# Optimization experiments

Measured on AMD Instinct MI355X. Metric: run time of the kernel, lower is better.

## Reference

```python
import jax, jax.numpy as jnp
import numpy as np

K = 1024
DIM = 64
DECAY = 0.99
EPS = 1e-05
CC = 0.25


def setup_inputs() -> dict:
    key = jax.random.key(0)
    k1, k2 = jax.random.split(key)
    inputs = jax.random.normal(k1, (32, DIM, 64, 64), dtype=jnp.float32)
    # embedding initialized uniform(-1/K, 1/K); ema_w starts as a copy
    emb_w = jax.random.uniform(k2, (K, DIM), dtype=jnp.float32, minval=-1.0 / K, maxval=1.0 / K)
    ema_w = emb_w
    ema_cluster_size = jnp.zeros((K,), dtype=jnp.float32)
    return {"inputs": inputs, "emb_w": emb_w, "ema_cluster_size": ema_cluster_size, "ema_w": ema_w}


def reference(inputs, emb_w, ema_cluster_size, ema_w):
    # NCHW -> NHWC
    x = jnp.transpose(inputs, (0, 2, 3, 1))  # [B,H,W,D]
    B, H, W, D = x.shape
    flat = x.reshape(-1, D)  # [N,D]
    # squared L2 distances: |f|^2 - 2 f.W^T + |w|^2
    d = (jnp.sum(flat * flat, axis=1, keepdims=True)
         - 2.0 * flat @ emb_w.T
         + jnp.sum(emb_w * emb_w, axis=1)[None, :])  # [N,K]
    idx = jnp.argmin(d, axis=1)  # [N]
    encodings = idx.reshape(B, H, W)
    quantized = emb_w[idx].reshape(B, H, W, D)

    # training-mode EMA update (matches one_hot.sum(0) and one_hot.T @ flatten)
    counts = jax.ops.segment_sum(jnp.ones_like(idx, dtype=jnp.float32), idx, num_segments=K)
    new_cs = ema_cluster_size * DECAY + (1.0 - DECAY) * counts
    n = jnp.sum(new_cs)
    new_cs = (new_cs + EPS) / (n + K * EPS) * n
    dw = jax.ops.segment_sum(flat, idx, num_segments=K)  # [K,D]
    new_ema_w = ema_w * DECAY + (1.0 - DECAY) * dw
    new_emb_w = new_ema_w / new_cs[:, None]

    e_latent_loss = jnp.mean((quantized - x) ** 2)  # both terms equal in value
    loss = e_latent_loss + CC * e_latent_loss
    # straight-through (value-equal in fwd)
    q_out = jnp.transpose(quantized, (0, 3, 1, 2))  # NHWC -> NCHW
    nll = jnp.ones((1,), dtype=jnp.float32)
    return q_out, encodings, loss, nll, new_cs, new_ema_w, new_emb_w
```

## Files before the change

kernel.cpp:

```cpp
#include <hip/hip_runtime.h>
#include <math.h>

#define KCODES 1024
#define DIMV   64
#define NROWS  131072
#define HWSZ   4096
#define NELEM  8388608
#define CAP    224
#define CANDCAP 1024


typedef __attribute__((ext_vector_type(8))) short bf16x8;
typedef __attribute__((ext_vector_type(4))) float f32x4;

static __device__ __forceinline__ unsigned short f2bf(float x) {
    unsigned int u = __float_as_uint(x);
    unsigned int r = (u + 0x7FFFu + ((u >> 16) & 1u)) >> 16;
    return (unsigned short)r;
}

__global__ __launch_bounds__(64) void vq_prep3_kernel(
    const float* __restrict__ emb, float* __restrict__ s_w,
    unsigned short* __restrict__ WB, unsigned int* __restrict__ wmax_bits)
{
    int k = blockIdx.x, t = threadIdx.x;
    float v = emb[k * DIMV + t];

    {
        int cg = k >> 4, n = k & 15;
        int kh = t >> 5, q = (t & 31) >> 3, j = t & 7;
        WB[((cg * 2 + kh) * 4 + q) * 128 + n * 8 + j] = f2bf(v);
    }

    float av = fabsf(v);
    #pragma unroll
    for (int off = 32; off > 0; off >>= 1)
        av = fmaxf(av, __shfl_down(av, off, 64));
    if (t == 0) atomicMax(wmax_bits, __float_as_uint(av));

    __shared__ float sv[64];
    __shared__ float sr[8];
    sv[t] = v;
    __syncthreads();
    if (t < 8) {
        float x = sv[t];
        float sq = x * x;
        asm("" : "+v"(sq));
        float r = sq;
        #pragma unroll
        for (int m = 1; m < 8; ++m) {
            float y = sv[8 * m + t];
            float s2 = y * y;
            asm("" : "+v"(s2));
            r += s2;
        }
        sr[t] = r;
    }
    __syncthreads();
    if (t == 0)
        s_w[k] = ((sr[0] + sr[1]) + (sr[2] + sr[3])) + ((sr[4] + sr[5]) + (sr[6] + sr[7]));
}

__global__ __launch_bounds__(256, 4) void vq_assign_kernel(
    const float* __restrict__ inp, const float* __restrict__ emb,
    const unsigned short* __restrict__ WB, const float* __restrict__ s_w,
    const unsigned int* __restrict__ wmax_bits,
    float* __restrict__ tmp_flat, float* __restrict__ enc_out,
    double* __restrict__ loss_sum, int* __restrict__ counts,
    int* __restrict__ rowlist)
{
    __shared__ float At[128 * 65];
    __shared__ float sfL[128];
    __shared__ float errL[128];
    __shared__ unsigned long long rowBest[128];
    __shared__ int bkL[128];
    __shared__ int candL[CANDCAP];
    __shared__ int candCnt;

    const int t = threadIdx.x;
    const int n0 = blockIdx.x * 128;
    const int bq  = n0 >> 12;
    const int hw0 = n0 & 4095;
    const float* fin = inp + (size_t)bq * (DIMV * HWSZ) + hw0;

    if (t < 128) rowBest[t] = ~0ULL;
    if (t == 0) candCnt = 0;

    #pragma unroll
    for (int j = 0; j < 8; ++j) {
        int id = j * 256 + t;
        int i = id >> 5;
        int c4 = id & 31;
        float4 v = *(const float4*)(fin + (size_t)i * HWSZ + 4 * c4);
        int r = 4 * c4;
        At[(r + 0) * 65 + i] = v.x + v.x;  At[(r + 1) * 65 + i] = v.y + v.y;
        At[(r + 2) * 65 + i] = v.z + v.z;  At[(r + 3) * 65 + i] = v.w + v.w;
    }
    __syncthreads();

    if (t < 128) {
        const float* gr = &At[t * 65];
        float r8[8];
        #pragma unroll
        for (int j = 0; j < 8; ++j) {
            float h = 0.5f * gr[j];
            float sq = h * h;
            asm("" : "+v"(sq));
            r8[j] = sq;
        }
        #pragma unroll
        for (int m = 1; m < 8; ++m) {
            #pragma unroll
            for (int j = 0; j < 8; ++j) {
                float h = 0.5f * gr[8 * m + j];
                float sq = h * h;
                asm("" : "+v"(sq));
                r8[j] += sq;
            }
        }
        sfL[t] = ((r8[0] + r8[1]) + (r8[2] + r8[3])) + ((r8[4] + r8[5]) + (r8[6] + r8[7]));
        float S = 0.0f;
        #pragma unroll
        for (int i = 0; i < 64; ++i) S += fabsf(gr[i]);
        float wmax = __uint_as_float(*wmax_bits);
        errL[t] = fmaf(S * wmax, 0.015625f, 2e-5f);
    }
    __syncthreads();

    const int wv = t >> 6, l = t & 63;
    const int m = l & 15, q = l >> 4;
    bf16x8 afr[2][2];
    float sfr[2][4];
    float erf[2][4];
    #pragma unroll
    for (int rg2 = 0; rg2 < 2; ++rg2) {
        int row = (2 * wv + rg2) * 16 + m;
        const float* gr = &At[row * 65];
        #pragma unroll
        for (int kh = 0; kh < 2; ++kh) {
            bf16x8 a;
            #pragma unroll
            for (int j = 0; j < 8; ++j)
                a[j] = (short)f2bf(gr[kh * 32 + q * 8 + j]);
            afr[rg2][kh] = a;
        }
        #pragma unroll
        for (int reg = 0; reg < 4; ++reg) {
            sfr[rg2][reg] = sfL[(2 * wv + rg2) * 16 + q * 4 + reg];
            erf[rg2][reg] = errL[(2 * wv + rg2) * 16 + q * 4 + reg];
        }
    }

    const unsigned short* wbq = WB + q * 128 + m * 8;
    const float* swm = s_w + m;

    float mn[2][4];
    #pragma unroll
    for (int rg2 = 0; rg2 < 2; ++rg2)
        #pragma unroll
        for (int reg = 0; reg < 4; ++reg) mn[rg2][reg] = 3.0e38f;

    {
        bf16x8 pa0 = *(const bf16x8*)(wbq);
        bf16x8 pa1 = *(const bf16x8*)(wbq + 512);
        float   swa = swm[0];
        bf16x8 pb0 = *(const bf16x8*)(wbq + 1024);
        bf16x8 pb1 = *(const bf16x8*)(wbq + 1024 + 512);
        float   swb = swm[16];
        for (int cg = 0; cg < 64; cg += 2) {
            #pragma unroll
            for (int rg2 = 0; rg2 < 2; ++rg2) {
                f32x4 acc = {0.f, 0.f, 0.f, 0.f};
                acc = __builtin_amdgcn_mfma_f32_16x16x32_bf16(afr[rg2][0], pa0, acc, 0, 0, 0);
                acc = __builtin_amdgcn_mfma_f32_16x16x32_bf16(afr[rg2][1], pa1, acc, 0, 0, 0);
                #pragma unroll
                for (int reg = 0; reg < 4; ++reg) {
                    float dt = (sfr[rg2][reg] - acc[reg]) + swa;
                    mn[rg2][reg] = fminf(mn[rg2][reg], dt);
                }
            }
            int cna = cg + 2 <= 62 ? cg + 2 : 62;
            pa0 = *(const bf16x8*)(wbq + cna * 1024);
            pa1 = *(const bf16x8*)(wbq + cna * 1024 + 512);
            swa = swm[cna * 16];
            #pragma unroll
            for (int rg2 = 0; rg2 < 2; ++rg2) {
                f32x4 acc = {0.f, 0.f, 0.f, 0.f};
                acc = __builtin_amdgcn_mfma_f32_16x16x32_bf16(afr[rg2][0], pb0, acc, 0, 0, 0);
                acc = __builtin_amdgcn_mfma_f32_16x16x32_bf16(afr[rg2][1], pb1, acc, 0, 0, 0);
                #pragma unroll
                for (int reg = 0; reg < 4; ++reg) {
                    float dt = (sfr[rg2][reg] - acc[reg]) + swb;
                    mn[rg2][reg] = fminf(mn[rg2][reg], dt);
                }
            }
            int cnb = cg + 3 <= 63 ? cg + 3 : 63;
            pb0 = *(const bf16x8*)(wbq + cnb * 1024);
            pb1 = *(const bf16x8*)(wbq + cnb * 1024 + 512);
            swb = swm[cnb * 16];
        }
    }

    float th[2][4];
    #pragma unroll
    for (int rg2 = 0; rg2 < 2; ++rg2)
        #pragma unroll
        for (int reg = 0; reg < 4; ++reg) {
            float v = mn[rg2][reg];
            v = fminf(v, __shfl_xor(v, 1, 64));
            v = fminf(v, __shfl_xor(v, 2, 64));
            v = fminf(v, __shfl_xor(v, 4, 64));
            v = fminf(v, __shfl_xor(v, 8, 64));
            th[rg2][reg] = v + erf[rg2][reg];
        }

    {
        bf16x8 pa0 = *(const bf16x8*)(wbq);
        bf16x8 pa1 = *(const bf16x8*)(wbq + 512);
        float   swa = swm[0];
        bf16x8 pb0 = *(const bf16x8*)(wbq + 1024);
        bf16x8 pb1 = *(const bf16x8*)(wbq + 1024 + 512);
        float   swb = swm[16];
        for (int cg = 0; cg < 64; cg += 2) {
            #pragma unroll
            for (int rg2 = 0; rg2 < 2; ++rg2) {
                f32x4 acc = {0.f, 0.f, 0.f, 0.f};
                acc = __builtin_amdgcn_mfma_f32_16x16x32_bf16(afr[rg2][0], pa0, acc, 0, 0, 0);
                acc = __builtin_amdgcn_mfma_f32_16x16x32_bf16(afr[rg2][1], pa1, acc, 0, 0, 0);
                #pragma unroll
                for (int reg = 0; reg < 4; ++reg) {
                    float dt = (sfr[rg2][reg] - acc[reg]) + swa;
                    if (dt <= th[rg2][reg]) {
                        int row = (2 * wv + rg2) * 16 + q * 4 + reg;
                        int p = atomicAdd(&candCnt, 1);
                        if (p < CANDCAP) candL[p] = (row << 10) | (cg * 16 + m);
                    }
                }
            }
            int cna = cg + 2 <= 62 ? cg + 2 : 62;
            pa0 = *(const bf16x8*)(wbq + cna * 1024);
            pa1 = *(const bf16x8*)(wbq + cna * 1024 + 512);
            swa = swm[cna * 16];
            #pragma unroll
            for (int rg2 = 0; rg2 < 2; ++rg2) {
                f32x4 acc = {0.f, 0.f, 0.f, 0.f};
                acc = __builtin_amdgcn_mfma_f32_16x16x32_bf16(afr[rg2][0], pb0, acc, 0, 0, 0);
                acc = __builtin_amdgcn_mfma_f32_16x16x32_bf16(afr[rg2][1], pb1, acc, 0, 0, 0);
                #pragma unroll
                for (int reg = 0; reg < 4; ++reg) {
                    float dt = (sfr[rg2][reg] - acc[reg]) + swb;
                    if (dt <= th[rg2][reg]) {
                        int row = (2 * wv + rg2) * 16 + q * 4 + reg;
                        int p = atomicAdd(&candCnt, 1);
                        if (p < CANDCAP) candL[p] = (row << 10) | ((cg + 1) * 16 + m);
                    }
                }
            }
            int cnb = cg + 3 <= 63 ? cg + 3 : 63;
            pb0 = *(const bf16x8*)(wbq + cnb * 1024);
            pb1 = *(const bf16x8*)(wbq + cnb * 1024 + 512);
            swb = swm[cnb * 16];
        }
    }
    __syncthreads();

    int nc = candCnt < CANDCAP ? candCnt : CANDCAP;
    for (int c = t; c < nc; c += 256) {
        int pk = candL[c];
        int r = pk >> 10, k = pk & 1023;
        const float* wk = emb + (size_t)k * DIMV;
        const float* gr = &At[r * 65];
        float acc = 0.0f;
        #pragma unroll
        for (int i = 0; i < DIMV; ++i)
            acc = __builtin_fmaf(gr[i], wk[i], acc);
        float d = (sfL[r] - acc) + s_w[k];
        unsigned int u = __float_as_uint(d);
        unsigned int s = (u & 0x80000000u) ? ~u : (u | 0x80000000u);
        unsigned long long key = ((unsigned long long)s << 32) | (unsigned int)k;
        atomicMin(&rowBest[r], key);
    }
    __syncthreads();

    if (t < 128 && (rowBest[t] == ~0ULL || candCnt > CANDCAP)) {
        int r = t;
        const float* gr = &At[r * 65];
        float bd = 3.0e38f; int bk = 0;
        for (int k = 0; k < KCODES; ++k) {
            const float* wk = emb + (size_t)k * DIMV;
            float acc = 0.0f;
            #pragma unroll
            for (int i = 0; i < DIMV; ++i)
                acc = __builtin_fmaf(gr[i], wk[i], acc);
            float d = (sfL[r] - acc) + s_w[k];
            if (d < bd) { bd = d; bk = k; }
        }
        unsigned int u = __float_as_uint(bd);
        unsigned int s = (u & 0x80000000u) ? ~u : (u | 0x80000000u);
        rowBest[r] = ((unsigned long long)s << 32) | (unsigned int)bk;
    }
    __syncthreads();

    if (t < 128) {
        int r = t;
        int bk = (int)(rowBest[r] & 1023ULL);
        enc_out[n0 + r] = (float)bk;
        bkL[r] = bk;
        int pos = atomicAdd(&counts[bk], 1);
        if (pos < CAP) rowlist[bk * CAP + pos] = n0 + r;
    }
    __syncthreads();

    float* tq = tmp_flat + (size_t)n0 * DIMV;
    double lsum = 0.0;
    #pragma unroll
    for (int j = 0; j < 32; ++j) {
        int idx = j * 256 + t;
        int r = idx >> 6;
        int i = idx & 63;
        int bk = bkL[r];
        float fi = 0.5f * At[r * 65 + i];
        tq[r * DIMV + i] = fi;
        float qv = emb[bk * DIMV + i];
        double dq = (double)qv - (double)fi;
        lsum = fma(dq, dq, lsum);
    }
    #pragma unroll
    for (int off = 32; off > 0; off >>= 1)
        lsum += __shfl_down(lsum, off, 64);
    if ((t & 63) == 0) atomicAdd(loss_sum, lsum);
}

__global__ __launch_bounds__(256) void vq_dw_all_kernel(
    const float* __restrict__ tmp_flat, const int* __restrict__ rowlist,
    const int* __restrict__ counts, const float* __restrict__ ema_cs,
    const float* __restrict__ ema_w, const double* __restrict__ loss_sum,
    float* __restrict__ out_loss, float* __restrict__ out_nll,
    float* __restrict__ out_ncs, float* __restrict__ out_nema,
    float* __restrict__ out_nemb)
{
    const int k = blockIdx.x;
    const int t = threadIdx.x;
    const double DECAY = 0.99;
    const double OMD   = 1.0 - 0.99;
    const double EPSV  = 1e-5;

    __shared__ double sm[256];
    double part = 0.0;
    #pragma unroll
    for (int j0 = 0; j0 < 4; ++j0) {
        int j = j0 * 256 + t;
        part += (double)ema_cs[j] * DECAY + OMD * (double)counts[j];
    }
    sm[t] = part;
    __syncthreads();
    #pragma unroll
    for (int off = 128; off > 0; off >>= 1) {
        if (t < off) sm[t] += sm[t + off];
        __syncthreads();
    }
    double nsum = sm[0];

    int cnt = counts[k];
    double ncs = (double)ema_cs[k] * DECAY + OMD * (double)cnt;
    double adj = (ncs + EPSV) / (nsum + (double)KCODES * EPSV) * nsum;
    if (t == 0) out_ncs[k] = (float)adj;
    if (k == 0 && t == 0) {
        double e = loss_sum[0] / (double)NELEM;
        out_loss[0] = (float)(e + 0.25 * e);
        out_nll[0]  = 1.0f;
    }

    int i = t & 63;
    int sub = t >> 6;
    int cap = cnt < CAP ? cnt : CAP;

    float acc = 0.0f;
    for (int r = sub; r < cap; r += 4) {
        int n = rowlist[k * CAP + r];
        acc += tmp_flat[(size_t)n * DIMV + i];
    }

    __shared__ float red[256];
    red[t] = acc;
    __syncthreads();
    if (t < 128) red[t] += red[t + 128];
    __syncthreads();
    if (t < 64) {
        float dwv = red[t] + red[t + 64];
        int idx = k * DIMV + i;
        double ne = (double)ema_w[idx] * DECAY + OMD * (double)dwv;
        out_nema[idx] = (float)ne;
        out_nemb[idx] = (float)(ne / adj);
    }
}

__global__ __launch_bounds__(256) void vq_qout_kernel(
    const float* __restrict__ enc, const float* __restrict__ emb,
    float* __restrict__ q_out)
{
    __shared__ int bkL[128];
    const int t = threadIdx.x;
    const int n0 = blockIdx.x * 128;
    const int bq  = n0 >> 12;
    const int hw0 = n0 & 4095;
    if (t < 128) bkL[t] = (int)enc[n0 + t];
    __syncthreads();
    float* qo = q_out + (size_t)bq * (DIMV * HWSZ) + hw0;
    #pragma unroll
    for (int j = 0; j < 32; ++j) {
        int idx = j * 256 + t;
        int r = idx & 127;
        int i = idx >> 7;
        qo[(size_t)i * HWSZ + r] = emb[bkL[r] * DIMV + i];
    }
}

extern "C" void kernel_launch(void* const* d_in, const int* in_sizes, int n_in,
                              void* d_out, int out_size, void* d_ws, size_t ws_size,
                              hipStream_t stream) {
    const float* inp    = (const float*)d_in[0];
    const float* emb    = (const float*)d_in[1];
    const float* ema_cs = (const float*)d_in[2];
    const float* ema_w  = (const float*)d_in[3];

    char* ws = (char*)d_ws;
    double*         loss_sum  = (double*)(ws + 0);
    unsigned int*   wmax_bits = (unsigned int*)(ws + 16);
    int*            counts    = (int*)(ws + 32);
    float*          s_w       = (float*)(ws + 4128);
    unsigned short* WB        = (unsigned short*)(ws + 8224);
    int*            rowlist   = (int*)(ws + 139296);

    float* out       = (float*)d_out;
    float* q_out     = out;
    float* enc_out   = out + 8388608;
    float* out_loss  = out + 8519680;
    float* out_nll   = out + 8519681;
    float* out_ncs   = out + 8519682;
    float* out_nema  = out + 8520706;
    float* out_nemb  = out + 8586242;

    hipMemsetAsync(ws, 0, 4128, stream);
    hipLaunchKernelGGL(vq_prep3_kernel, dim3(KCODES), dim3(64), 0, stream,
                       emb, s_w, WB, wmax_bits);
    hipLaunchKernelGGL(vq_assign_kernel, dim3(NROWS / 128), dim3(256), 0, stream,
                       inp, emb, WB, s_w, wmax_bits,
                       q_out , enc_out, loss_sum, counts, rowlist);
    hipLaunchKernelGGL(vq_dw_all_kernel, dim3(KCODES), dim3(256), 0, stream,
                       q_out , rowlist, counts, ema_cs, ema_w, loss_sum,
                       out_loss, out_nll, out_ncs, out_nema, out_nemb);
    hipLaunchKernelGGL(vq_qout_kernel, dim3(NROWS / 128), dim3(256), 0, stream,
                       enc_out, emb, q_out);
}
```

Baseline: 278.8 us.

## Halve rows per block in VQ assign kernel and drop per-row norm from distance

The assign kernel now handles 64 rows per block instead of 128, with each wave owning a single 16-row MFMA tile. This halves the A-fragment and min registers and lets the launch bound ask for 8 blocks per CU. The row norm |f|^2 is removed from the per-code distance compare, since it is constant per row and does not change the argmin or the threshold test. The candidate buffer shrinks, and the dw gather loop gets an unroll hint. The trade-off is that every block now reloads the full codebook for half as many rows, doubling codebook traffic through L2.

```diff
diff --git a/kernel.cpp b/kernel.cpp
--- a/kernel.cpp
+++ b/kernel.cpp
@@ -7,7 +7,8 @@
 #define HWSZ   4096
 #define NELEM  8388608
 #define CAP    224
-#define CANDCAP 1024
+#define CANDCAP 384
+#define RPB    64
 
 
 typedef __attribute__((ext_vector_type(8))) short bf16x8;
@@ -61,7 +62,7 @@
         s_w[k] = ((sr[0] + sr[1]) + (sr[2] + sr[3])) + ((sr[4] + sr[5]) + (sr[6] + sr[7]));
 }
 
-__global__ __launch_bounds__(256, 4) void vq_assign_kernel(
+__global__ __launch_bounds__(256, 8) void vq_assign_kernel(
     const float* __restrict__ inp, const float* __restrict__ emb,
     const unsigned short* __restrict__ WB, const float* __restrict__ s_w,
     const unsigned int* __restrict__ wmax_bits,
@@ -69,28 +70,28 @@
     double* __restrict__ loss_sum, int* __restrict__ counts,
     int* __restrict__ rowlist)
 {
-    __shared__ float At[128 * 65];
-    __shared__ float sfL[128];
-    __shared__ float errL[128];
-    __shared__ unsigned long long rowBest[128];
-    __shared__ int bkL[128];
+    __shared__ float At[RPB * 65];
+    __shared__ float sfL[RPB];
+    __shared__ float errL[RPB];
+    __shared__ unsigned long long rowBest[RPB];
+    __shared__ int bkL[RPB];
     __shared__ int candL[CANDCAP];
     __shared__ int candCnt;
 
     const int t = threadIdx.x;
-    const int n0 = blockIdx.x * 128;
+    const int n0 = blockIdx.x * RPB;
     const int bq  = n0 >> 12;
     const int hw0 = n0 & 4095;
     const float* fin = inp + (size_t)bq * (DIMV * HWSZ) + hw0;
 
-    if (t < 128) rowBest[t] = ~0ULL;
+    if (t < RPB) rowBest[t] = ~0ULL;
     if (t == 0) candCnt = 0;
 
     #pragma unroll
-    for (int j = 0; j < 8; ++j) {
+    for (int j = 0; j < 4; ++j) {
         int id = j * 256 + t;
-        int i = id >> 5;
-        int c4 = id & 31;
+        int i = id >> 4;
+        int c4 = id & 15;
         float4 v = *(const float4*)(fin + (size_t)i * HWSZ + 4 * c4);
         int r = 4 * c4;
         At[(r + 0) * 65 + i] = v.x + v.x;  At[(r + 1) * 65 + i] = v.y + v.y;
@@ -98,7 +99,7 @@
     }
     __syncthreads();
 
-    if (t < 128) {
+    if (t < RPB) {
         const float* gr = &At[t * 65];
         float r8[8];
         #pragma unroll
@@ -129,36 +130,22 @@
 
     const int wv = t >> 6, l = t & 63;
     const int m = l & 15, q = l >> 4;
-    bf16x8 afr[2][2];
-    float sfr[2][4];
-    float erf[2][4];
-    #pragma unroll
-    for (int rg2 = 0; rg2 < 2; ++rg2) {
-        int row = (2 * wv + rg2) * 16 + m;
+    bf16x8 a0, a1;
+    {
+        int row = wv * 16 + m;
         const float* gr = &At[row * 65];
         #pragma unroll
-        for (int kh = 0; kh < 2; ++kh) {
-            bf16x8 a;
-            #pragma unroll
-            for (int j = 0; j < 8; ++j)
-                a[j] = (short)f2bf(gr[kh * 32 + q * 8 + j]);
-            afr[rg2][kh] = a;
-        }
-        #pragma unroll
-        for (int reg = 0; reg < 4; ++reg) {
-            sfr[rg2][reg] = sfL[(2 * wv + rg2) * 16 + q * 4 + reg];
-            erf[rg2][reg] = errL[(2 * wv + rg2) * 16 + q * 4 + reg];
-        }
+        for (int j = 0; j < 8; ++j) a0[j] = (short)f2bf(gr[q * 8 + j]);
+        #pragma unroll
+        for (int j = 0; j < 8; ++j) a1[j] = (short)f2bf(gr[32 + q * 8 + j]);
     }
 
     const unsigned short* wbq = WB + q * 128 + m * 8;
     const float* swm = s_w + m;
 
-    float mn[2][4];
-    #pragma unroll
-    for (int rg2 = 0; rg2 < 2; ++rg2)
-        #pragma unroll
-        for (int reg = 0; reg < 4; ++reg) mn[rg2][reg] = 3.0e38f;
+    float mn[4];
+    #pragma unroll
+    for (int reg = 0; reg < 4; ++reg) mn[reg] = 3.0e38f;
 
     {
         bf16x8 pa0 = *(const bf16x8*)(wbq);
@@ -168,51 +155,43 @@
         bf16x8 pb1 = *(const bf16x8*)(wbq + 1024 + 512);
         float   swb = swm[16];
         for (int cg = 0; cg < 64; cg += 2) {
-            #pragma unroll
-            for (int rg2 = 0; rg2 < 2; ++rg2) {
+            {
                 f32x4 acc = {0.f, 0.f, 0.f, 0.f};
-                acc = __builtin_amdgcn_mfma_f32_16x16x32_bf16(afr[rg2][0], pa0, acc, 0, 0, 0);
-                acc = __builtin_amdgcn_mfma_f32_16x16x32_bf16(afr[rg2][1], pa1, acc, 0, 0, 0);
+                acc = __builtin_amdgcn_mfma_f32_16x16x32_bf16(a0, pa0, acc, 0, 0, 0);
+                acc = __builtin_amdgcn_mfma_f32_16x16x32_bf16(a1, pa1, acc, 0, 0, 0);
                 #pragma unroll
-                for (int reg = 0; reg < 4; ++reg) {
-                    float dt = (sfr[rg2][reg] - acc[reg]) + swa;
-                    mn[rg2][reg] = fminf(mn[rg2][reg], dt);
-                }
+                for (int reg = 0; reg < 4; ++reg)
+                    mn[reg] = fminf(mn[reg], swa - acc[reg]);
             }
-            int cna = cg + 2 <= 62 ? cg + 2 : 62;
+            int cna = (cg + 2) & 63;
             pa0 = *(const bf16x8*)(wbq + cna * 1024);
             pa1 = *(const bf16x8*)(wbq + cna * 1024 + 512);
             swa = swm[cna * 16];
-            #pragma unroll
-            for (int rg2 = 0; rg2 < 2; ++rg2) {
+            {
                 f32x4 acc = {0.f, 0.f, 0.f, 0.f};
-                acc = __builtin_amdgcn_mfma_f32_16x16x32_bf16(afr[rg2][0], pb0, acc, 0, 0, 0);
-                acc = __builtin_amdgcn_mfma_f32_16x16x32_bf16(afr[rg2][1], pb1, acc, 0, 0, 0);
+                acc = __builtin_amdgcn_mfma_f32_16x16x32_bf16(a0, pb0, acc, 0, 0, 0);
+                acc = __builtin_amdgcn_mfma_f32_16x16x32_bf16(a1, pb1, acc, 0, 0, 0);
                 #pragma unroll
-                for (int reg = 0; reg < 4; ++reg) {
-                    float dt = (sfr[rg2][reg] - acc[reg]) + swb;
-                    mn[rg2][reg] = fminf(mn[rg2][reg], dt);
-                }
+                for (int reg = 0; reg < 4; ++reg)
+                    mn[reg] = fminf(mn[reg], swb - acc[reg]);
             }
-            int cnb = cg + 3 <= 63 ? cg + 3 : 63;
+            int cnb = (cg + 3) & 63;
             pb0 = *(const bf16x8*)(wbq + cnb * 1024);
             pb1 = *(const bf16x8*)(wbq + cnb * 1024 + 512);
             swb = swm[cnb * 16];
         }
     }
 
-    float th[2][4];
-    #pragma unroll
-    for (int rg2 = 0; rg2 < 2; ++rg2)
-        #pragma unroll
-        for (int reg = 0; reg < 4; ++reg) {
-            float v = mn[rg2][reg];
-            v = fminf(v, __shfl_xor(v, 1, 64));
-            v = fminf(v, __shfl_xor(v, 2, 64));
-            v = fminf(v, __shfl_xor(v, 4, 64));
-            v = fminf(v, __shfl_xor(v, 8, 64));
-            th[rg2][reg] = v + erf[rg2][reg];
-        }
+    float th[4];
+    #pragma unroll
+    for (int reg = 0; reg < 4; ++reg) {
+        float v = mn[reg];
+        v = fminf(v, __shfl_xor(v, 1, 64));
+        v = fminf(v, __shfl_xor(v, 2, 64));
+        v = fminf(v, __shfl_xor(v, 4, 64));
+        v = fminf(v, __shfl_xor(v, 8, 64));
+        th[reg] = v + errL[wv * 16 + q * 4 + reg];
+    }
 
     {
         bf16x8 pa0 = *(const bf16x8*)(wbq);
@@ -222,41 +201,37 @@
         bf16x8 pb1 = *(const bf16x8*)(wbq + 1024 + 512);
         float   swb = swm[16];
         for (int cg = 0; cg < 64; cg += 2) {
-            #pragma unroll
-            for (int rg2 = 0; rg2 < 2; ++rg2) {
+            {
                 f32x4 acc = {0.f, 0.f, 0.f, 0.f};
-                acc = __builtin_amdgcn_mfma_f32_16x16x32_bf16(afr[rg2][0], pa0, acc, 0, 0, 0);
-                acc = __builtin_amdgcn_mfma_f32_16x16x32_bf16(afr[rg2][1], pa1, acc, 0, 0, 0);
+                acc = __builtin_amdgcn_mfma_f32_16x16x32_bf16(a0, pa0, acc, 0, 0, 0);
+                acc = __builtin_amdgcn_mfma_f32_16x16x32_bf16(a1, pa1, acc, 0, 0, 0);
                 #pragma unroll
                 for (int reg = 0; reg < 4; ++reg) {
-                    float dt = (sfr[rg2][reg] - acc[reg]) + swa;
-                    if (dt <= th[rg2][reg]) {
-                        int row = (2 * wv + rg2) * 16 + q * 4 + reg;
+                    if (swa - acc[reg] <= th[reg]) {
+                        int row = wv * 16 + q * 4 + reg;
                         int p = atomicAdd(&candCnt, 1);
                         if (p < CANDCAP) candL[p] = (row << 10) | (cg * 16 + m);
                     }
                 }
             }
-            int cna = cg + 2 <= 62 ? cg + 2 : 62;
+            int cna = (cg + 2) & 63;
             pa0 = *(const bf16x8*)(wbq + cna * 1024);
             pa1 = *(const bf16x8*)(wbq + cna * 1024 + 512);
             swa = swm[cna * 16];
-            #pragma unroll
-            for (int rg2 = 0; rg2 < 2; ++rg2) {
+            {
                 f32x4 acc = {0.f, 0.f, 0.f, 0.f};
-                acc = __builtin_amdgcn_mfma_f32_16x16x32_bf16(afr[rg2][0], pb0, acc, 0, 0, 0);
-                acc = __builtin_amdgcn_mfma_f32_16x16x32_bf16(afr[rg2][1], pb1, acc, 0, 0, 0);
+                acc = __builtin_amdgcn_mfma_f32_16x16x32_bf16(a0, pb0, acc, 0, 0, 0);
+                acc = __builtin_amdgcn_mfma_f32_16x16x32_bf16(a1, pb1, acc, 0, 0, 0);
                 #pragma unroll
                 for (int reg = 0; reg < 4; ++reg) {
-                    float dt = (sfr[rg2][reg] - acc[reg]) + swb;
-                    if (dt <= th[rg2][reg]) {
-                        int row = (2 * wv + rg2) * 16 + q * 4 + reg;
+                    if (swb - acc[reg] <= th[reg]) {
+                        int row = wv * 16 + q * 4 + reg;
                         int p = atomicAdd(&candCnt, 1);
                         if (p < CANDCAP) candL[p] = (row << 10) | ((cg + 1) * 16 + m);
                     }
                 }
             }
-            int cnb = cg + 3 <= 63 ? cg + 3 : 63;
+            int cnb = (cg + 3) & 63;
             pb0 = *(const bf16x8*)(wbq + cnb * 1024);
             pb1 = *(const bf16x8*)(wbq + cnb * 1024 + 512);
             swb = swm[cnb * 16];
@@ -282,7 +257,7 @@
     }
     __syncthreads();
 
-    if (t < 128 && (rowBest[t] == ~0ULL || candCnt > CANDCAP)) {
+    if (t < RPB && (rowBest[t] == ~0ULL || candCnt > CANDCAP)) {
         int r = t;
         const float* gr = &At[r * 65];
         float bd = 3.0e38f; int bk = 0;
@@ -301,7 +276,7 @@
     }
     __syncthreads();
 
-    if (t < 128) {
+    if (t < RPB) {
         int r = t;
         int bk = (int)(rowBest[r] & 1023ULL);
         enc_out[n0 + r] = (float)bk;
@@ -314,7 +289,7 @@
     float* tq = tmp_flat + (size_t)n0 * DIMV;
     double lsum = 0.0;
     #pragma unroll
-    for (int j = 0; j < 32; ++j) {
+    for (int j = 0; j < 16; ++j) {
         int idx = j * 256 + t;
         int r = idx >> 6;
         int i = idx & 63;
@@ -376,6 +351,7 @@
     int cap = cnt < CAP ? cnt : CAP;
 
     float acc = 0.0f;
+    #pragma unroll 4
     for (int r = sub; r < cap; r += 4) {
         int n = rowlist[k * CAP + r];
         acc += tmp_flat[(size_t)n * DIMV + i];
@@ -444,7 +420,7 @@
     hipMemsetAsync(ws, 0, 4128, stream);
     hipLaunchKernelGGL(vq_prep3_kernel, dim3(KCODES), dim3(64), 0, stream,
                        emb, s_w, WB, wmax_bits);
-    hipLaunchKernelGGL(vq_assign_kernel, dim3(NROWS / 128), dim3(256), 0, stream,
+    hipLaunchKernelGGL(vq_assign_kernel, dim3(NROWS / RPB), dim3(256), 0, stream,
                        inp, emb, WB, s_w, wmax_bits,
                        q_out , enc_out, loss_sum, counts, rowlist);
     hipLaunchKernelGGL(vq_dw_all_kernel, dim3(KCODES), dim3(256), 0, stream,
```

Measured after the change: 334.9 us. 20.1% more time.

## Stage codebook tiles through double-buffered LDS in VQ assign kernel

Applied to the files above, without the earlier changes.

Replaces per-lane global loads of the bf16 codebook with cooperative block-wide staging into a double-buffered LDS tile, prefetching the next tile into registers during MFMA work. Also caches the code-norm vector in LDS and drops the per-row |f|^2 term from the min-search, since it is constant per row and does not change the argmin. The extra LDS lowers the occupancy hint from 4 to 3 blocks per CU and adds two barriers per tile pair. The dw kernel also gets an unroll pragma.

```diff
diff --git a/kernel.cpp b/kernel.cpp
--- a/kernel.cpp
+++ b/kernel.cpp
@@ -8,6 +8,7 @@
 #define NELEM  8388608
 #define CAP    224
 #define CANDCAP 1024
+#define RPB    128
 
 
 typedef __attribute__((ext_vector_type(8))) short bf16x8;
@@ -61,7 +62,7 @@
         s_w[k] = ((sr[0] + sr[1]) + (sr[2] + sr[3])) + ((sr[4] + sr[5]) + (sr[6] + sr[7]));
 }
 
-__global__ __launch_bounds__(256, 4) void vq_assign_kernel(
+__global__ __launch_bounds__(256, 3) void vq_assign_kernel(
     const float* __restrict__ inp, const float* __restrict__ emb,
     const unsigned short* __restrict__ WB, const float* __restrict__ s_w,
     const unsigned int* __restrict__ wmax_bits,
@@ -69,22 +70,27 @@
     double* __restrict__ loss_sum, int* __restrict__ counts,
     int* __restrict__ rowlist)
 {
-    __shared__ float At[128 * 65];
-    __shared__ float sfL[128];
-    __shared__ float errL[128];
-    __shared__ unsigned long long rowBest[128];
-    __shared__ int bkL[128];
+    __shared__ float At[RPB * 65];
+    __shared__ float sWL[KCODES];
+    __shared__ __align__(16) unsigned short Bst[2][2048];
+    __shared__ float sfL[RPB];
+    __shared__ float errL[RPB];
+    __shared__ unsigned long long rowBest[RPB];
+    __shared__ int bkL[RPB];
     __shared__ int candL[CANDCAP];
     __shared__ int candCnt;
 
     const int t = threadIdx.x;
-    const int n0 = blockIdx.x * 128;
+    const int n0 = blockIdx.x * RPB;
     const int bq  = n0 >> 12;
     const int hw0 = n0 & 4095;
     const float* fin = inp + (size_t)bq * (DIMV * HWSZ) + hw0;
 
-    if (t < 128) rowBest[t] = ~0ULL;
+    if (t < RPB) rowBest[t] = ~0ULL;
     if (t == 0) candCnt = 0;
+
+    #pragma unroll
+    for (int j = 0; j < 4; ++j) sWL[j * 256 + t] = s_w[j * 256 + t];
 
     #pragma unroll
     for (int j = 0; j < 8; ++j) {
@@ -96,9 +102,17 @@
         At[(r + 0) * 65 + i] = v.x + v.x;  At[(r + 1) * 65 + i] = v.y + v.y;
         At[(r + 2) * 65 + i] = v.z + v.z;  At[(r + 3) * 65 + i] = v.w + v.w;
     }
-    __syncthreads();
-
-    if (t < 128) {
+
+    const uint4* wbsrc = (const uint4*)WB;
+    uint4 nx0, nx1;
+    {
+        uint4 st0 = wbsrc[t];
+        *(uint4*)&Bst[0][t * 8] = st0;
+        nx0 = wbsrc[256 + t];
+    }
+    __syncthreads();
+
+    if (t < RPB) {
         const float* gr = &At[t * 65];
         float r8[8];
         #pragma unroll
@@ -129,8 +143,8 @@
 
     const int wv = t >> 6, l = t & 63;
     const int m = l & 15, q = l >> 4;
+    const int lq = q * 128 + m * 8;
     bf16x8 afr[2][2];
-    float sfr[2][4];
     float erf[2][4];
     #pragma unroll
     for (int rg2 = 0; rg2 < 2; ++rg2) {
@@ -145,14 +159,9 @@
             afr[rg2][kh] = a;
         }
         #pragma unroll
-        for (int reg = 0; reg < 4; ++reg) {
-            sfr[rg2][reg] = sfL[(2 * wv + rg2) * 16 + q * 4 + reg];
+        for (int reg = 0; reg < 4; ++reg)
             erf[rg2][reg] = errL[(2 * wv + rg2) * 16 + q * 4 + reg];
-        }
-    }
-
-    const unsigned short* wbq = WB + q * 128 + m * 8;
-    const float* swm = s_w + m;
+    }
 
     float mn[2][4];
     #pragma unroll
@@ -160,45 +169,47 @@
         #pragma unroll
         for (int reg = 0; reg < 4; ++reg) mn[rg2][reg] = 3.0e38f;
 
-    {
-        bf16x8 pa0 = *(const bf16x8*)(wbq);
-        bf16x8 pa1 = *(const bf16x8*)(wbq + 512);
-        float   swa = swm[0];
-        bf16x8 pb0 = *(const bf16x8*)(wbq + 1024);
-        bf16x8 pb1 = *(const bf16x8*)(wbq + 1024 + 512);
-        float   swb = swm[16];
-        for (int cg = 0; cg < 64; cg += 2) {
+    #pragma unroll 1
+    for (int tp = 0; tp < 16; ++tp) {
+        int tt = 2 * tp;
+        nx1 = wbsrc[((tt + 2) & 31) * 256 + t];
+        #pragma unroll
+        for (int c = 0; c < 2; ++c) {
+            int cg = 2 * tt + c;
+            bf16x8 b0 = *(const bf16x8*)&Bst[0][c * 1024 + lq];
+            bf16x8 b1 = *(const bf16x8*)&Bst[0][c * 1024 + 512 + lq];
+            float sw = sWL[cg * 16 + m];
             #pragma unroll
             for (int rg2 = 0; rg2 < 2; ++rg2) {
                 f32x4 acc = {0.f, 0.f, 0.f, 0.f};
-                acc = __builtin_amdgcn_mfma_f32_16x16x32_bf16(afr[rg2][0], pa0, acc, 0, 0, 0);
-                acc = __builtin_amdgcn_mfma_f32_16x16x32_bf16(afr[rg2][1], pa1, acc, 0, 0, 0);
+                acc = __builtin_amdgcn_mfma_f32_16x16x32_bf16(afr[rg2][0], b0, acc, 0, 0, 0);
+                acc = __builtin_amdgcn_mfma_f32_16x16x32_bf16(afr[rg2][1], b1, acc, 0, 0, 0);
                 #pragma unroll
-                for (int reg = 0; reg < 4; ++reg) {
-                    float dt = (sfr[rg2][reg] - acc[reg]) + swa;
-                    mn[rg2][reg] = fminf(mn[rg2][reg], dt);
-                }
+                for (int reg = 0; reg < 4; ++reg)
+                    mn[rg2][reg] = fminf(mn[rg2][reg], sw - acc[reg]);
             }
-            int cna = cg + 2 <= 62 ? cg + 2 : 62;
-            pa0 = *(const bf16x8*)(wbq + cna * 1024);
-            pa1 = *(const bf16x8*)(wbq + cna * 1024 + 512);
-            swa = swm[cna * 16];
+        }
+        *(uint4*)&Bst[1][t * 8] = nx0;
+        __syncthreads();
+        nx0 = wbsrc[((tt + 3) & 31) * 256 + t];
+        #pragma unroll
+        for (int c = 0; c < 2; ++c) {
+            int cg = 2 * (tt + 1) + c;
+            bf16x8 b0 = *(const bf16x8*)&Bst[1][c * 1024 + lq];
+            bf16x8 b1 = *(const bf16x8*)&Bst[1][c * 1024 + 512 + lq];
+            float sw = sWL[cg * 16 + m];
             #pragma unroll
             for (int rg2 = 0; rg2 < 2; ++rg2) {
                 f32x4 acc = {0.f, 0.f, 0.f, 0.f};
-                acc = __builtin_amdgcn_mfma_f32_16x16x32_bf16(afr[rg2][0], pb0, acc, 0, 0, 0);
-                acc = __builtin_amdgcn_mfma_f32_16x16x32_bf16(afr[rg2][1], pb1, acc, 0, 0, 0);
+                acc = __builtin_amdgcn_mfma_f32_16x16x32_bf16(afr[rg2][0], b0, acc, 0, 0, 0);
+                acc = __builtin_amdgcn_mfma_f32_16x16x32_bf16(afr[rg2][1], b1, acc, 0, 0, 0);
                 #pragma unroll
-                for (int reg = 0; reg < 4; ++reg) {
-                    float dt = (sfr[rg2][reg] - acc[reg]) + swb;
-                    mn[rg2][reg] = fminf(mn[rg2][reg], dt);
-                }
+                for (int reg = 0; reg < 4; ++reg)
+                    mn[rg2][reg] = fminf(mn[rg2][reg], sw - acc[reg]);
             }
-            int cnb = cg + 3 <= 63 ? cg + 3 : 63;
-            pb0 = *(const bf16x8*)(wbq + cnb * 1024);
-            pb1 = *(const bf16x8*)(wbq + cnb * 1024 + 512);
-            swb = swm[cnb * 16];
-        }
+        }
+        *(uint4*)&Bst[0][t * 8] = nx1;
+        __syncthreads();
     }
 
     float th[2][4];
@@ -214,55 +225,58 @@
             th[rg2][reg] = v + erf[rg2][reg];
         }
 
-    {
-        bf16x8 pa0 = *(const bf16x8*)(wbq);
-        bf16x8 pa1 = *(const bf16x8*)(wbq + 512);
-        float   swa = swm[0];
-        bf16x8 pb0 = *(const bf16x8*)(wbq + 1024);
-        bf16x8 pb1 = *(const bf16x8*)(wbq + 1024 + 512);
-        float   swb = swm[16];
-        for (int cg = 0; cg < 64; cg += 2) {
+    #pragma unroll 1
+    for (int tp = 0; tp < 16; ++tp) {
+        int tt = 2 * tp;
+        nx1 = wbsrc[((tt + 2) & 31) * 256 + t];
+        #pragma unroll
+        for (int c = 0; c < 2; ++c) {
+            int cg = 2 * tt + c;
+            bf16x8 b0 = *(const bf16x8*)&Bst[0][c * 1024 + lq];
+            bf16x8 b1 = *(const bf16x8*)&Bst[0][c * 1024 + 512 + lq];
+            float sw = sWL[cg * 16 + m];
             #pragma unroll
             for (int rg2 = 0; rg2 < 2; ++rg2) {
                 f32x4 acc = {0.f, 0.f, 0.f, 0.f};
-                acc = __builtin_amdgcn_mfma_f32_16x16x32_bf16(afr[rg2][0], pa0, acc, 0, 0, 0);
-                acc = __builtin_amdgcn_mfma_f32_16x16x32_bf16(afr[rg2][1], pa1, acc, 0, 0, 0);
+                acc = __builtin_amdgcn_mfma_f32_16x16x32_bf16(afr[rg2][0], b0, acc, 0, 0, 0);
+                acc = __builtin_amdgcn_mfma_f32_16x16x32_bf16(afr[rg2][1], b1, acc, 0, 0, 0);
                 #pragma unroll
                 for (int reg = 0; reg < 4; ++reg) {
-                    float dt = (sfr[rg2][reg] - acc[reg]) + swa;
-                    if (dt <= th[rg2][reg]) {
+                    if (sw - acc[reg] <= th[rg2][reg]) {
                         int row = (2 * wv + rg2) * 16 + q * 4 + reg;
                         int p = atomicAdd(&candCnt, 1);
                         if (p < CANDCAP) candL[p] = (row << 10) | (cg * 16 + m);
                     }
                 }
             }
-            int cna = cg + 2 <= 62 ? cg + 2 : 62;
-            pa0 = *(const bf16x8*)(wbq + cna * 1024);
-            pa1 = *(const bf16x8*)(wbq + cna * 1024 + 512);
-            swa = swm[cna * 16];
+        }
+        *(uint4*)&Bst[1][t * 8] = nx0;
+        __syncthreads();
+        nx0 = wbsrc[((tt + 3) & 31) * 256 + t];
+        #pragma unroll
+        for (int c = 0; c < 2; ++c) {
+            int cg = 2 * (tt + 1) + c;
+            bf16x8 b0 = *(const bf16x8*)&Bst[1][c * 1024 + lq];
+            bf16x8 b1 = *(const bf16x8*)&Bst[1][c * 1024 + 512 + lq];
+            float sw = sWL[cg * 16 + m];
             #pragma unroll
             for (int rg2 = 0; rg2 < 2; ++rg2) {
                 f32x4 acc = {0.f, 0.f, 0.f, 0.f};
-                acc = __builtin_amdgcn_mfma_f32_16x16x32_bf16(afr[rg2][0], pb0, acc, 0, 0, 0);
-                acc = __builtin_amdgcn_mfma_f32_16x16x32_bf16(afr[rg2][1], pb1, acc, 0, 0, 0);
+                acc = __builtin_amdgcn_mfma_f32_16x16x32_bf16(afr[rg2][0], b0, acc, 0, 0, 0);
+                acc = __builtin_amdgcn_mfma_f32_16x16x32_bf16(afr[rg2][1], b1, acc, 0, 0, 0);
                 #pragma unroll
                 for (int reg = 0; reg < 4; ++reg) {
-                    float dt = (sfr[rg2][reg] - acc[reg]) + swb;
-                    if (dt <= th[rg2][reg]) {
+                    if (sw - acc[reg] <= th[rg2][reg]) {
                         int row = (2 * wv + rg2) * 16 + q * 4 + reg;
                         int p = atomicAdd(&candCnt, 1);
-                        if (p < CANDCAP) candL[p] = (row << 10) | ((cg + 1) * 16 + m);
+                        if (p < CANDCAP) candL[p] = (row << 10) | (cg * 16 + m);
                     }
                 }
             }
-            int cnb = cg + 3 <= 63 ? cg + 3 : 63;
-            pb0 = *(const bf16x8*)(wbq + cnb * 1024);
-            pb1 = *(const bf16x8*)(wbq + cnb * 1024 + 512);
-            swb = swm[cnb * 16];
-        }
-    }
-    __syncthreads();
+        }
+        *(uint4*)&Bst[0][t * 8] = nx1;
+        __syncthreads();
+    }
 
     int nc = candCnt < CANDCAP ? candCnt : CANDCAP;
     for (int c = t; c < nc; c += 256) {
@@ -274,7 +288,7 @@
         #pragma unroll
         for (int i = 0; i < DIMV; ++i)
             acc = __builtin_fmaf(gr[i], wk[i], acc);
-        float d = (sfL[r] - acc) + s_w[k];
+        float d = (sfL[r] - acc) + sWL[k];
         unsigned int u = __float_as_uint(d);
         unsigned int s = (u & 0x80000000u) ? ~u : (u | 0x80000000u);
         unsigned long long key = ((unsigned long long)s << 32) | (unsigned int)k;
@@ -282,7 +296,7 @@
     }
     __syncthreads();
 
-    if (t < 128 && (rowBest[t] == ~0ULL || candCnt > CANDCAP)) {
+    if (t < RPB && (rowBest[t] == ~0ULL || candCnt > CANDCAP)) {
         int r = t;
         const float* gr = &At[r * 65];
         float bd = 3.0e38f; int bk = 0;
@@ -292,7 +306,7 @@
             #pragma unroll
             for (int i = 0; i < DIMV; ++i)
                 acc = __builtin_fmaf(gr[i], wk[i], acc);
-            float d = (sfL[r] - acc) + s_w[k];
+            float d = (sfL[r] - acc) + sWL[k];
             if (d < bd) { bd = d; bk = k; }
         }
         unsigned int u = __float_as_uint(bd);
@@ -301,7 +315,7 @@
     }
     __syncthreads();
 
-    if (t < 128) {
+    if (t < RPB) {
         int r = t;
         int bk = (int)(rowBest[r] & 1023ULL);
         enc_out[n0 + r] = (float)bk;
@@ -376,6 +390,7 @@
     int cap = cnt < CAP ? cnt : CAP;
 
     float acc = 0.0f;
+    #pragma unroll 4
     for (int r = sub; r < cap; r += 4) {
         int n = rowlist[k * CAP + r];
         acc += tmp_flat[(size_t)n * DIMV + i];
@@ -444,7 +459,7 @@
     hipMemsetAsync(ws, 0, 4128, stream);
     hipLaunchKernelGGL(vq_prep3_kernel, dim3(KCODES), dim3(64), 0, stream,
                        emb, s_w, WB, wmax_bits);
-    hipLaunchKernelGGL(vq_assign_kernel, dim3(NROWS / 128), dim3(256), 0, stream,
+    hipLaunchKernelGGL(vq_assign_kernel, dim3(NROWS / RPB), dim3(256), 0, stream,
                        inp, emb, WB, s_w, wmax_bits,
                        q_out , enc_out, loss_sum, counts, rowlist);
     hipLaunchKernelGGL(vq_dw_all_kernel, dim3(KCODES), dim3(256), 0, stream,
```

After: 266.4 us. 4.4% less time.
